# Kernel optimization log

Hardware: AMD Instinct MI355X
Metric: run time of the kernel (lower is better)

Reference implementation:

```python
import jax, jax.numpy as jnp
import numpy as np

N, K, M, H, F = 4, 1024, 1024, 16, 4096
D = M // H  # per-head dim (dim_q = dim_v = 64)
EPS = 1e-5


def _mha(q_in, k_in, v_in, Wq, bq, Wk, bk, Wv, bv, Wo, bo, mask):
    # Wq/Wk/Wv: [H, M, D]; bq/bk/bv: [H, D]; Wo: [H*D, M]; bo: [M]
    q = jnp.einsum('nkm,hmd->nhkd', q_in, Wq) + bq[None, :, None, :]
    k = jnp.einsum('nkm,hmd->nhkd', k_in, Wk) + bk[None, :, None, :]
    v = jnp.einsum('nkm,hmd->nhkd', v_in, Wv) + bv[None, :, None, :]
    scores = jnp.einsum('nhkd,nhld->nhkl', q, k) / jnp.sqrt(jnp.asarray(D, q.dtype))
    if mask is not None:
        scores = jnp.where(mask[:, None, :, :] == 0, jnp.asarray(-jnp.inf, q.dtype), scores)
    attn = jax.nn.softmax(scores, axis=-1)          # [N,H,K,K]
    y = jnp.einsum('nhkl,nhld->nhkd', attn, v)      # [N,H,K,D]
    y = y.transpose(0, 2, 1, 3).reshape(q_in.shape[0], q_in.shape[1], -1)  # concat heads -> [N,K,H*D]
    return y @ Wo + bo


def _ln(x, g, b):
    mu = jnp.mean(x, axis=-1, keepdims=True)
    var = jnp.mean((x - mu) ** 2, axis=-1, keepdims=True)
    return (x - mu) * jax.lax.rsqrt(var + EPS) * g + b


def setup_inputs() -> dict:
    key = jax.random.key(0)
    ks = jax.random.split(key, 24)
    s = 0.02
    def rn(k, shape):
        return jax.random.normal(k, shape, dtype=jnp.float32) * s
    inp = {
        'dec_inp': jax.random.normal(ks[0], (N, K, M), dtype=jnp.float32),
        'enc_out': jax.random.normal(ks[1], (N, K, M), dtype=jnp.float32),
        'mask': jnp.tril(jnp.ones((K, K), dtype=jnp.int32))[None].repeat(N, axis=0),
        # self-attention params
        'Wq_s': rn(ks[2], (H, M, D)), 'bq_s': jnp.zeros((H, D)),
        'Wk_s': rn(ks[3], (H, M, D)), 'bk_s': jnp.zeros((H, D)),
        'Wv_s': rn(ks[4], (H, M, D)), 'bv_s': jnp.zeros((H, D)),
        'Wo_s': rn(ks[5], (H * D, M)), 'bo_s': jnp.zeros((M,)),
        # cross-attention params
        'Wq_c': rn(ks[6], (H, M, D)), 'bq_c': jnp.zeros((H, D)),
        'Wk_c': rn(ks[7], (H, M, D)), 'bk_c': jnp.zeros((H, D)),
        'Wv_c': rn(ks[8], (H, M, D)), 'bv_c': jnp.zeros((H, D)),
        'Wo_c': rn(ks[9], (H * D, M)), 'bo_c': jnp.zeros((M,)),
        # feedforward params
        'W1': rn(ks[10], (M, F)), 'b1': jnp.zeros((F,)),
        'W2': rn(ks[11], (F, M)), 'b2': jnp.zeros((M,)),
        # layernorm params
        'g1': jnp.ones((M,)), 'be1': jnp.zeros((M,)),
        'g2': jnp.ones((M,)), 'be2': jnp.zeros((M,)),
        'g3': jnp.ones((M,)), 'be3': jnp.zeros((M,)),
    }
    return inp


def reference(dec_inp, enc_out, mask,
              Wq_s, bq_s, Wk_s, bk_s, Wv_s, bv_s, Wo_s, bo_s,
              Wq_c, bq_c, Wk_c, bk_c, Wv_c, bv_c, Wo_c, bo_c,
              W1, b1, W2, b2, g1, be1, g2, be2, g3, be3):
    # masked self-attention + residual + LN (dropout = identity in eval)
    out1 = _mha(dec_inp, dec_inp, dec_inp, Wq_s, bq_s, Wk_s, bk_s, Wv_s, bv_s, Wo_s, bo_s, mask)
    out2 = _ln(dec_inp + out1, g1, be1)
    # cross-attention with encoder output + residual + LN
    out3 = _mha(out2, enc_out, enc_out, Wq_c, bq_c, Wk_c, bk_c, Wv_c, bv_c, Wo_c, bo_c, None)
    out4 = _ln(out3 + out2, g2, be2)
    # feedforward + residual + LN
    out5 = jax.nn.relu(out4 @ W1 + b1) @ W2 + b2
    return _ln(out5 + out4, g3, be3)
```

## Files before the change

kernel.cpp:

```cpp
#include <hip/hip_runtime.h>

#define NB   4
#define SEQ  1024
#define MD   1024
#define NH   16
#define HD   64
#define FF   4096
#define NK   (NB*SEQ)
#define EPSF 1e-5f
#define QS   3072

typedef short short8 __attribute__((ext_vector_type(8)));
typedef float f32x4  __attribute__((ext_vector_type(4)));
typedef unsigned short u16;
typedef unsigned int u32;

__device__ __forceinline__ u16 f2bf(float x) {
    union { float f; unsigned u; } v; v.f = x;
    unsigned r = v.u + 0x7FFF + ((v.u >> 16) & 1);
    return (u16)(r >> 16);
}
__device__ __forceinline__ u16 f2bf_trunc(float x) {
    union { float f; unsigned u; } v; v.f = x;
    return (u16)(v.u >> 16);
}
__device__ __forceinline__ float bf2f(u16 x) {
    union { unsigned u; float f; } v; v.u = ((unsigned)x) << 16;
    return v.f;
}
__device__ __forceinline__ void gload_lds16(const void* g, void* l) {
    __builtin_amdgcn_global_load_lds(
        (const __attribute__((address_space(1))) unsigned int*)g,
        (__attribute__((address_space(3))) unsigned int*)l,
        16, 0, 0);
}

__global__ __launch_bounds__(256) void conv_bf16(const float* __restrict__ s0,
                                                 const float* __restrict__ s1,
                                                 u16* __restrict__ d0,
                                                 u16* __restrict__ d1) {
    const float* S = blockIdx.y ? s1 : s0;
    u16* D = blockIdx.y ? d1 : d0;
    const int i = blockIdx.x * 256 + threadIdx.x;
    float4 v = ((const float4*)S)[i];
    ushort4 o;
    o.x = f2bf(v.x); o.y = f2bf(v.y); o.z = f2bf(v.z); o.w = f2bf(v.w);
    ((ushort4*)D)[i] = o;
}

__global__ __launch_bounds__(256) void mask_tiles(const int* __restrict__ mask,
                                                  int* __restrict__ cls,
                                                  u32* __restrict__ bits) {
    const int jt = blockIdx.x, qt = blockIdx.y, n = blockIdx.z;
    const int t = threadIdx.x;
    const int r = t >> 1, h2 = (t & 1) * 2;
    u32 bb[2];
#pragma unroll
    for (int sg = 0; sg < 2; ++sg) {
        const int* mp = &mask[((size_t)n * SEQ + qt * 128 + r) * SEQ + jt * 128 + (h2 + sg) * 32];
        u32 b = 0;
#pragma unroll
        for (int k = 0; k < 8; ++k) {
            int4 v = *(const int4*)(mp + k * 4);
            b |= (v.x ? 1u : 0u) << (k * 4 + 0);
            b |= (v.y ? 1u : 0u) << (k * 4 + 1);
            b |= (v.z ? 1u : 0u) << (k * 4 + 2);
            b |= (v.w ? 1u : 0u) << (k * 4 + 3);
        }
        bb[sg] = b;
    }
    const int tile = (n * 8 + qt) * 8 + jt;
    bits[((size_t)tile * 128 + r) * 4 + h2]     = bb[0];
    bits[((size_t)tile * 128 + r) * 4 + h2 + 1] = bb[1];
    const int nfull  = __syncthreads_count(bb[0] == 0xFFFFFFFFu && bb[1] == 0xFFFFFFFFu);
    const int nempty = __syncthreads_count(bb[0] == 0u && bb[1] == 0u);
    if (t == 0) cls[tile] = (nfull == 256) ? 2 : ((nempty == 256) ? 0 : 1);
}

struct QkvArgs { const float* src[6]; u16* dst[6]; };

__global__ __launch_bounds__(256) void repack_qkv(QkvArgs a) {
    const int m0 = blockIdx.x * 64;
    const int h  = blockIdx.y;
    const int w  = blockIdx.z;
    const float* W = a.src[w];
    u16* BT = a.dst[w];
    const int t = threadIdx.x;
    __shared__ u16 Ts[64][72];

    const int r = t >> 4, c4 = (t & 15) * 4;
#pragma unroll
    for (int p = 0; p < 4; ++p) {
        const int row = r + p * 16;
        float4 v = *(const float4*)&W[((size_t)h * 1024 + m0 + row) * 64 + c4];
        Ts[row][c4] = f2bf(v.x); Ts[row][c4 + 1] = f2bf(v.y);
        Ts[row][c4 + 2] = f2bf(v.z); Ts[row][c4 + 3] = f2bf(v.w);
    }
    __syncthreads();
    const int d = t >> 2, j0 = (t & 3) * 16;
#pragma unroll
    for (int p = 0; p < 4; ++p) {
        ushort4 o;
        o.x = Ts[j0 + p * 4 + 0][d]; o.y = Ts[j0 + p * 4 + 1][d];
        o.z = Ts[j0 + p * 4 + 2][d]; o.w = Ts[j0 + p * 4 + 3][d];
        *(ushort4*)&BT[((size_t)h * 64 + d) * 1024 + m0 + j0 + p * 4] = o;
    }
}

struct FD { const float* src; int ss; u16* dst; int ds; };
struct FlatArgs { FD d[10]; };

__global__ __launch_bounds__(256) void repack_flat(FlatArgs fa) {
    FD u = fa.d[blockIdx.z];
    const int r0 = blockIdx.x * 64;
    const int c0 = blockIdx.y * 64;
    const int t  = threadIdx.x;
    __shared__ u16 Ts[64][72];

    const int r = t >> 4, c4 = (t & 15) * 4;
#pragma unroll
    for (int p = 0; p < 4; ++p) {
        const int row = r + p * 16;
        float4 v = *(const float4*)&u.src[(size_t)(r0 + row) * u.ss + c0 + c4];
        Ts[row][c4] = f2bf(v.x); Ts[row][c4 + 1] = f2bf(v.y);
        Ts[row][c4 + 2] = f2bf(v.z); Ts[row][c4 + 3] = f2bf(v.w);
    }
    __syncthreads();
    const int d = t >> 2, j0 = (t & 3) * 16;
#pragma unroll
    for (int p = 0; p < 4; ++p) {
        ushort4 o;
        o.x = Ts[j0 + p * 4 + 0][d]; o.y = Ts[j0 + p * 4 + 1][d];
        o.z = Ts[j0 + p * 4 + 2][d]; o.w = Ts[j0 + p * 4 + 3][d];
        *(ushort4*)&u.dst[(size_t)(c0 + d) * u.ds + r0 + j0 + p * 4] = o;
    }
}

template<int OUT_BF16, int RELU, int RESID, int BIAS3, int PARTIAL, int VT>
__global__ __launch_bounds__(256) void gemm_mfma(const u16* __restrict__ A,
                                                 const u16* __restrict__ A2,
                                                 int Astride,
                                                 const u16* __restrict__ BT,
                                                 int Bstride,
                                                 const float* __restrict__ b0,
                                                 const float* __restrict__ b1p,
                                                 const float* __restrict__ b2p,
                                                 const float* __restrict__ resid,
                                                 void* __restrict__ Cout,
                                                 u16* __restrict__ VtOut,
                                                 int Kd, int Nd) {
    const int nt = blockIdx.x;
    const int mt = blockIdx.y;
    const int t  = threadIdx.x;
    const int wave = t >> 6, lane = t & 63;
    const int q = lane >> 4, l16 = lane & 15;
    const int wm = wave >> 1, wn = wave & 1;

    __shared__ __align__(16) u16 As[128 * 64];
    __shared__ __align__(16) u16 Bs[128 * 64];

    const int row0 = mt * 128, col0 = nt * 128;
    const u16* Ause = (col0 < 1024) ? A : A2;
    const int kBase = PARTIAL ? blockIdx.z * Kd : 0;

    f32x4 acc[4][4];
#pragma unroll
    for (int r = 0; r < 4; ++r)
#pragma unroll
        for (int c = 0; c < 4; ++c) acc[r][c] = (f32x4)0.0f;

    const int lrow = lane >> 3;
    const int lcb  = lane & 7;

    for (int k0 = 0; k0 < Kd; k0 += 64) {
        __syncthreads();
#pragma unroll
        for (int p = 0; p < 4; ++p) {
            const int rr = wave * 32 + p * 8 + lrow;
            const int gcb = lcb ^ (rr & 7);
            gload_lds16(Ause + (size_t)(row0 + rr) * Astride + kBase + k0 + gcb * 8, As + (size_t)(wave * 32 + p * 8) * 64);
            gload_lds16(BT   + (size_t)(col0 + rr) * Bstride + kBase + k0 + gcb * 8, Bs + (size_t)(wave * 32 + p * 8) * 64);
        }
        __syncthreads();

#pragma unroll
        for (int s = 0; s < 2; ++s) {
            const int pb = (q + s * 4) ^ (l16 & 7);
            short8 af[4], bf[4];
#pragma unroll
            for (int r = 0; r < 4; ++r)
                af[r] = *(const short8*)&As[(wm * 64 + r * 16 + l16) * 64 + pb * 8];
#pragma unroll
            for (int c = 0; c < 4; ++c)
                bf[c] = *(const short8*)&Bs[(wn * 64 + c * 16 + l16) * 64 + pb * 8];
#pragma unroll
            for (int r = 0; r < 4; ++r)
#pragma unroll
                for (int c = 0; c < 4; ++c)
                    acc[r][c] = __builtin_amdgcn_mfma_f32_16x16x32_bf16(af[r], bf[c], acc[r][c], 0, 0, 0);
        }
    }

    float* Pout = PARTIAL ? ((float*)Cout + (size_t)blockIdx.z * NK * Nd) : nullptr;

#pragma unroll
    for (int c = 0; c < 4; ++c) {
        const int col = col0 + wn * 64 + c * 16 + l16;
        float bb = 0.0f;
        if (!PARTIAL) {
            if (BIAS3) {
                const int sec = col >> 10;
                const float* bp = sec == 0 ? b0 : (sec == 1 ? b1p : b2p);
                bb = bp[col & 1023];
            } else {
                bb = b0[col];
            }
        }
#pragma unroll
        for (int r = 0; r < 4; ++r) {
#pragma unroll
            for (int reg = 0; reg < 4; ++reg) {
                const int row = row0 + wm * 64 + r * 16 + q * 4 + reg;
                float v = acc[r][c][reg] + bb;
                if (PARTIAL) {
                    Pout[(size_t)row * Nd + col] = acc[r][c][reg];
                } else {
                    if (RELU)  v = fmaxf(v, 0.0f);
                    if (RESID) v += resid[(size_t)row * Nd + col];
                    if (OUT_BF16) ((u16*)Cout)[(size_t)row * Nd + col] = f2bf(v);
                    else          ((float*)Cout)[(size_t)row * Nd + col] = v;
                }
            }
        }
    }
}

template<int BN, int OUT_BF16, int RELU, int BIAS3, int PARTIAL, int VT>
__global__ __launch_bounds__(512, 2) void gemm256(const u16* __restrict__ A,
                                                  const u16* __restrict__ A2,
                                                  int Astride,
                                                  const u16* __restrict__ BT,
                                                  int Bstride,
                                                  const float* __restrict__ b0,
                                                  const float* __restrict__ b1p,
                                                  const float* __restrict__ b2p,
                                                  void* __restrict__ Cout,
                                                  u16* __restrict__ VtOut,
                                                  int Kd, int Nd, int swzW) {
    const int t  = threadIdx.x;
    const int wave = t >> 6, lane = t & 63;
    const int q = lane >> 4, l16 = lane & 15;
    const int wm = wave >> 2, wn = wave & 3;
    constexpr int NC = BN / 64;

    const int gx = gridDim.x;
    const int bid = blockIdx.x + blockIdx.y * gx;
    const int cpx = (gx * gridDim.y) >> 3;
    const int xcd = bid & 7;
    const int cc  = bid >> 3;
    const int regNX = gx / swzW;
    const int mtspan = cpx / swzW;
    const int nt = (xcd % regNX) * swzW + cc % swzW;
    const int mt = (xcd / regNX) * mtspan + cc / swzW;

    extern __shared__ __align__(16) char smem[];
    u16* As = (u16*)smem;
    u16* Bs = (u16*)(smem + 2 * 256 * 64 * 2);

    const int row0 = mt * 256, col0 = nt * BN;
    const u16* Ause = (col0 < 1024) ? A : A2;
    const int kBase = PARTIAL ? blockIdx.z * Kd : 0;

    f32x4 acc[8][NC];
#pragma unroll
    for (int r = 0; r < 8; ++r)
#pragma unroll
        for (int c = 0; c < NC; ++c) acc[r][c] = (f32x4)0.0f;

    const int lrow = lane >> 3;
    const int lcb  = lane & 7;

    auto stage = [&](int buf, int kk) {
#pragma unroll
        for (int p = 0; p < 4; ++p) {
            const int rr = wave * 32 + p * 8 + lrow;
            const int gcb = lcb ^ (rr & 7);
            gload_lds16(Ause + (size_t)(row0 + rr) * Astride + kk + gcb * 8,
                        As + (size_t)buf * (256 * 64) + (wave * 32 + p * 8) * 64);
        }
#pragma unroll
        for (int p = 0; p < BN / 64; ++p) {
            const int rr = wave * (BN / 8) + p * 8 + lrow;
            const int gcb = lcb ^ (rr & 7);
            gload_lds16(BT + (size_t)(col0 + rr) * Bstride + kk + gcb * 8,
                        Bs + (size_t)buf * (BN * 64) + (wave * (BN / 8) + p * 8) * 64);
        }
    };

    const int nsteps = Kd / 64;
    stage(0, kBase);

    int cur = 0;
    for (int it = 0; it < nsteps; ++it) {
        const bool pre = (it + 1 < nsteps);
        if (pre) {
            stage(cur ^ 1, kBase + (it + 1) * 64);
            if constexpr (BN == 256) asm volatile("s_waitcnt vmcnt(8)" ::: "memory");
            else                     asm volatile("s_waitcnt vmcnt(6)" ::: "memory");
        } else {
            asm volatile("s_waitcnt vmcnt(0)" ::: "memory");
        }
        __builtin_amdgcn_s_barrier();

        const u16* Ab = As + (size_t)cur * (256 * 64);
        const u16* Bb = Bs + (size_t)cur * (BN * 64);
#pragma unroll
        for (int s = 0; s < 2; ++s) {
            const int pb = (q + s * 4) ^ (l16 & 7);
            short8 af[8], bf[NC];
#pragma unroll
            for (int r = 0; r < 8; ++r)
                af[r] = *(const short8*)&Ab[(wm * 128 + r * 16 + l16) * 64 + pb * 8];
#pragma unroll
            for (int c = 0; c < NC; ++c)
                bf[c] = *(const short8*)&Bb[(wn * (BN / 4) + c * 16 + l16) * 64 + pb * 8];
#pragma unroll
            for (int r = 0; r < 8; ++r)
#pragma unroll
                for (int c = 0; c < NC; ++c)
                    acc[r][c] = __builtin_amdgcn_mfma_f32_16x16x32_bf16(af[r], bf[c], acc[r][c], 0, 0, 0);
        }
        __builtin_amdgcn_s_barrier();
        cur ^= 1;
    }

    if (VT && col0 >= 2048) {
#pragma unroll
        for (int c = 0; c < NC; ++c) {
            const int col = col0 + wn * (BN / 4) + c * 16 + l16;
            const float bb = b2p[col & 1023];
            const int d = col & 63, hh = (col >> 6) & 15;
#pragma unroll
            for (int r = 0; r < 8; ++r) {
                const int row = row0 + wm * 128 + r * 16 + q * 4;
                const int nn = row >> 10, k = row & 1023;
                ushort4 o;
                o.x = f2bf(acc[r][c][0] + bb);
                o.y = f2bf(acc[r][c][1] + bb);
                o.z = f2bf(acc[r][c][2] + bb);
                o.w = f2bf(acc[r][c][3] + bb);
                *(ushort4*)&VtOut[((size_t)(nn * 16 + hh) * 64 + d) * 1024 + k] = o;
            }
        }
        return;
    }

    float* Pout = PARTIAL ? ((float*)Cout + (size_t)blockIdx.z * NK * Nd) : nullptr;

#pragma unroll
    for (int c = 0; c < NC; ++c) {
        const int col = col0 + wn * (BN / 4) + c * 16 + l16;
        float bb = 0.0f;
        if (!PARTIAL) {
            if (BIAS3) {
                const int sec = col >> 10;
                const float* bp = sec == 0 ? b0 : (sec == 1 ? b1p : b2p);
                bb = bp[col & 1023];
            } else {
                bb = b0[col];
            }
        }
#pragma unroll
        for (int r = 0; r < 8; ++r) {
#pragma unroll
            for (int reg = 0; reg < 4; ++reg) {
                const int row = row0 + wm * 128 + r * 16 + q * 4 + reg;
                float v = acc[r][c][reg] + bb;
                if (PARTIAL) {
                    Pout[(size_t)row * Nd + col] = acc[r][c][reg];
                } else {
                    if (RELU)  v = fmaxf(v, 0.0f);
                    if (OUT_BF16) ((u16*)Cout)[(size_t)row * Nd + col] = f2bf(v);
                    else          ((float*)Cout)[(size_t)row * Nd + col] = v;
                }
            }
        }
    }
}

#define PSTR 136
#define ATTN_LDS (128*64*2 + 64*128*2 + 8*16*PSTR*2)

__global__ __launch_bounds__(512, 4) void attn_mfma(const u16* __restrict__ QKV,
                                                    const u16* __restrict__ Vt,
                                                    const int* __restrict__ cls,
                                                    const u32* __restrict__ bits,
                                                    u16* __restrict__ Yout) {
    const int qt = blockIdx.x;
    const int h  = blockIdx.y;
    const int n  = blockIdx.z;
    const int t  = threadIdx.x;
    const int wave = t >> 6;
    const int lane = t & 63;
    const int quad = lane >> 4;
    const int l16  = lane & 15;
    const int sw   = wave >> 2;
    const int wq   = wave & 3;

    extern __shared__ __align__(16) char smem[];
    u16* Ks = (u16*)smem;
    u16* Vs = (u16*)(smem + 128 * 64 * 2);
    u16* Pw = (u16*)(smem + 128 * 64 * 2 + 64 * 128 * 2) + wave * 16 * PSTR;

    const int bh = n * NH + h;
    const int i0 = qt * 128;

    int cl[8];
    if (cls) {
        const int* cp = &cls[(n * 8 + qt) * 8];
#pragma unroll
        for (int j = 0; j < 8; ++j) cl[j] = cp[j];
    } else {
#pragma unroll
        for (int j = 0; j < 8; ++j) cl[j] = 2;
    }

    short8 qf[2];
    {
        const u16* qrow = QKV + ((size_t)n * SEQ + i0 + sw * 64 + wq * 16 + l16) * QS + h * 64 + quad * 8;
        short8 a = *(const short8*)(qrow);
        short8 b = *(const short8*)(qrow + 32);
#pragma unroll
        for (int j = 0; j < 8; ++j) {
            qf[0][j] = (short)f2bf(bf2f((u16)a[j]) * 0.18033688f);
            qf[1][j] = (short)f2bf(bf2f((u16)b[j]) * 0.18033688f);
        }
    }

    f32x4 O[4];
#pragma unroll
    for (int d = 0; d < 4; ++d) O[d] = (f32x4)0.0f;
    float lrow[4] = {};

    const int krow = lane >> 3, kblk = lane & 7;
    const int vrow = lane >> 4, vblk = lane & 15;
    const int x7 = l16 & 7;

    for (int jt = 0; jt < SEQ / 128; ++jt) {
        const int c = cl[jt];
        if (c == 0) continue;
        __syncthreads();

#pragma unroll
        for (int p = 0; p < 2; ++p) {
            const int rr = wave * 16 + p * 8 + krow;
            const int kb = kblk ^ (rr & 7);
            gload_lds16(QKV + ((size_t)n * SEQ + jt * 128 + rr) * QS + 1024 + h * 64 + kb * 8,
                        Ks + (wave * 16 + p * 8) * 64);
        }
#pragma unroll
        for (int p = 0; p < 2; ++p) {
            const int rr = wave * 8 + p * 4 + vrow;
            const int kb = vblk ^ (rr & 15);
            gload_lds16(Vt + ((size_t)bh * HD + rr) * SEQ + jt * 128 + kb * 8,
                        Vs + (wave * 8 + p * 4) * 128);
        }
        __syncthreads();

        f32x4 S[8];
#pragma unroll
        for (int sub = 0; sub < 8; ++sub) {
            S[sub] = (f32x4)0.0f;
            const int row = sub * 16 + l16;
            short8 k0 = *(const short8*)&Ks[row * 64 + ((quad ^ x7) * 8)];
            S[sub] = __builtin_amdgcn_mfma_f32_16x16x32_bf16(qf[0], k0, S[sub], 0, 0, 0);
            short8 k1 = *(const short8*)&Ks[row * 64 + (((4 + quad) ^ x7) * 8)];
            S[sub] = __builtin_amdgcn_mfma_f32_16x16x32_bf16(qf[1], k1, S[sub], 0, 0, 0);
        }

        if (c == 1) {
#pragma unroll
            for (int reg = 0; reg < 4; ++reg) {
                const int row = sw * 64 + wq * 16 + quad * 4 + reg;
                const uint4 mm = *(const uint4*)&bits[((size_t)((n * 8 + qt) * 8 + jt) * 128 + row) * 4];
#pragma unroll
                for (int sub = 0; sub < 8; ++sub) {
                    const u32 seg = (sub >> 1) == 0 ? mm.x : (sub >> 1) == 1 ? mm.y : (sub >> 1) == 2 ? mm.z : mm.w;
                    if (!((seg >> ((sub & 1) * 16 + l16)) & 1u)) S[sub][reg] = -1e30f;
                }
            }
        }

#pragma unroll
        for (int reg = 0; reg < 4; ++reg) {
            float rs = 0.0f;
#pragma unroll
            for (int sub = 0; sub < 8; ++sub) {
                float e = exp2f(S[sub][reg]);
                Pw[(quad * 4 + reg) * PSTR + sub * 16 + l16] = f2bf_trunc(e);
                rs += e;
            }
            rs += __shfl_xor(rs, 1);
            rs += __shfl_xor(rs, 2);
            rs += __shfl_xor(rs, 4);
            rs += __shfl_xor(rs, 8);
            lrow[reg] += rs;
        }

        short8 pa[4];
#pragma unroll
        for (int ks = 0; ks < 4; ++ks)
            pa[ks] = *(const short8*)&Pw[l16 * PSTR + ks * 32 + quad * 8];
#pragma unroll
        for (int d = 0; d < 4; ++d) {
            const int row = d * 16 + l16;
#pragma unroll
            for (int ks = 0; ks < 4; ++ks) {
                short8 vb = *(const short8*)&Vs[row * 128 + (((ks * 4 + quad) ^ l16) & 15) * 8];
                O[d] = __builtin_amdgcn_mfma_f32_16x16x32_bf16(pa[ks], vb, O[d], 0, 0, 0);
            }
        }
    }

#pragma unroll
    for (int d = 0; d < 4; ++d) {
#pragma unroll
        for (int reg = 0; reg < 4; ++reg) {
            const int row = i0 + sw * 64 + wq * 16 + quad * 4 + reg;
            const int col = h * 64 + d * 16 + l16;
            Yout[((size_t)n * SEQ + row) * QS + col] = f2bf(O[d][reg] / lrow[reg]);
        }
    }
}

__global__ __launch_bounds__(256) void ln_kernel(const float* __restrict__ X,
                                                 const float* __restrict__ g,
                                                 const float* __restrict__ be,
                                                 float* __restrict__ Y,
                                                 u16* __restrict__ Yb) {
    const int row = blockIdx.x;
    const int t = threadIdx.x;
    __shared__ float red[256];

    const float4 v = ((const float4*)(X + (size_t)row * MD))[t];
    red[t] = v.x + v.y + v.z + v.w;
    __syncthreads();
    for (int s2 = 128; s2 > 0; s2 >>= 1) {
        if (t < s2) red[t] += red[t + s2];
        __syncthreads();
    }
    const float mu = red[0] * (1.0f / MD);
    __syncthreads();

    float dx = v.x - mu, dy = v.y - mu, dz = v.z - mu, dw = v.w - mu;
    red[t] = dx * dx + dy * dy + dz * dz + dw * dw;
    __syncthreads();
    for (int s2 = 128; s2 > 0; s2 >>= 1) {
        if (t < s2) red[t] += red[t + s2];
        __syncthreads();
    }
    const float var = red[0] * (1.0f / MD);
    const float rs = rsqrtf(var + EPSF);

    const float4 gv = ((const float4*)g)[t];
    const float4 bv = ((const float4*)be)[t];
    float4 o;
    o.x = dx * rs * gv.x + bv.x;
    o.y = dy * rs * gv.y + bv.y;
    o.z = dz * rs * gv.z + bv.z;
    o.w = dw * rs * gv.w + bv.w;
    if (Y) ((float4*)(Y + (size_t)row * MD))[t] = o;
    if (Yb) {
        ushort4 ob;
        ob.x = f2bf(o.x); ob.y = f2bf(o.y); ob.z = f2bf(o.z); ob.w = f2bf(o.w);
        ((ushort4*)(Yb + (size_t)row * MD))[t] = ob;
    }
}

__global__ __launch_bounds__(256) void ln_fused2(const float* __restrict__ p0,
                                                 const float* __restrict__ p1,
                                                 const float* __restrict__ bias,
                                                 const float* __restrict__ resid,
                                                 const float* __restrict__ g,
                                                 const float* __restrict__ be,
                                                 float* __restrict__ Y) {
    const int row = blockIdx.x;
    const int t = threadIdx.x;
    __shared__ float red[256];

    const float4 a = ((const float4*)(p0 + (size_t)row * MD))[t];
    const float4 b = ((const float4*)(p1 + (size_t)row * MD))[t];
    const float4 r = ((const float4*)(resid + (size_t)row * MD))[t];
    const float4 bi = ((const float4*)bias)[t];
    float4 v;
    v.x = a.x + b.x + r.x + bi.x;
    v.y = a.y + b.y + r.y + bi.y;
    v.z = a.z + b.z + r.z + bi.z;
    v.w = a.w + b.w + r.w + bi.w;

    red[t] = v.x + v.y + v.z + v.w;
    __syncthreads();
    for (int s2 = 128; s2 > 0; s2 >>= 1) {
        if (t < s2) red[t] += red[t + s2];
        __syncthreads();
    }
    const float mu = red[0] * (1.0f / MD);
    __syncthreads();

    float dx = v.x - mu, dy = v.y - mu, dz = v.z - mu, dw = v.w - mu;
    red[t] = dx * dx + dy * dy + dz * dz + dw * dw;
    __syncthreads();
    for (int s2 = 128; s2 > 0; s2 >>= 1) {
        if (t < s2) red[t] += red[t + s2];
        __syncthreads();
    }
    const float var = red[0] * (1.0f / MD);
    const float rs = rsqrtf(var + EPSF);

    const float4 gv = ((const float4*)g)[t];
    const float4 bv = ((const float4*)be)[t];
    float4 o;
    o.x = dx * rs * gv.x + bv.x;
    o.y = dy * rs * gv.y + bv.y;
    o.z = dz * rs * gv.z + bv.z;
    o.w = dw * rs * gv.w + bv.w;
    ((float4*)(Y + (size_t)row * MD))[t] = o;
}

extern "C" void kernel_launch(void* const* d_in, const int* in_sizes, int n_in,
                              void* d_out, int out_size, void* d_ws, size_t ws_size,
                              hipStream_t stream) {
    const float* dec  = (const float*)d_in[0];
    const float* enc  = (const float*)d_in[1];
    const int*   mask = (const int*)d_in[2];
    const float* Wq_s = (const float*)d_in[3];
    const float* bq_s = (const float*)d_in[4];
    const float* Wk_s = (const float*)d_in[5];
    const float* bk_s = (const float*)d_in[6];
    const float* Wv_s = (const float*)d_in[7];
    const float* bv_s = (const float*)d_in[8];
    const float* Wo_s = (const float*)d_in[9];
    const float* bo_s = (const float*)d_in[10];
    const float* Wq_c = (const float*)d_in[11];
    const float* bq_c = (const float*)d_in[12];
    const float* Wk_c = (const float*)d_in[13];
    const float* bk_c = (const float*)d_in[14];
    const float* Wv_c = (const float*)d_in[15];
    const float* bv_c = (const float*)d_in[16];
    const float* Wo_c = (const float*)d_in[17];
    const float* bo_c = (const float*)d_in[18];
    const float* W1   = (const float*)d_in[19];
    const float* b1   = (const float*)d_in[20];
    const float* W2   = (const float*)d_in[21];
    const float* b2   = (const float*)d_in[22];
    const float* g1   = (const float*)d_in[23];
    const float* be1  = (const float*)d_in[24];
    const float* g2   = (const float*)d_in[25];
    const float* be2  = (const float*)d_in[26];
    const float* g3   = (const float*)d_in[27];
    const float* be3  = (const float*)d_in[28];

    char* wsb = (char*)d_ws;
    const size_t MB = 1u << 20;
    u16*   decb  = (u16*)(wsb + 0 * MB);
    u16*   O2b   = (u16*)(wsb + 0 * MB);
    u16*   encb  = (u16*)(wsb + 8 * MB);
    u16*   O4b   = (u16*)(wsb + 8 * MB);
    u16*   WqkvsT= (u16*)(wsb + 16 * MB);
    u16*   WqkvcT= (u16*)(wsb + 22 * MB);
    u16*   WosT  = (u16*)(wsb + 28 * MB);
    u16*   WocT  = (u16*)(wsb + 30 * MB);
    u16*   W1T   = (u16*)(wsb + 32 * MB);
    u16*   W2T   = (u16*)(wsb + 40 * MB);
    u16*   QKVb  = (u16*)(wsb + 48 * MB);
    u16*   Vt    = (u16*)(wsb + 72 * MB);
    u16*   Hb    = (u16*)(wsb + 48 * MB);
    int*   mcls  = (int*)(wsb + 80 * MB);
    u32*   mbits = (u32*)(wsb + 80 * MB + 64 * 1024);
    float* Tb    = (float*)(wsb + 80 * MB);
    float* FP    = (float*)(wsb + 0 * MB);
    float* O2    = (float*)(wsb + 96 * MB);
    float* O4    = (float*)(wsb + 96 * MB);

    dim3 blk(256);
    dim3 blkA(512);
    dim3 blkG(512);
    dim3 gConv(NK * MD / 4 / 256, 2);
    dim3 gMask(8, 8, 4);
    dim3 gQkvW(16, 16, 6);
    dim3 gFlatW(16, 16, 10);
    dim3 gAttn(SEQ / 128, NH, NB);
    dim3 gQKV(QS / 256, NK / 256);
    dim3 gOut(MD / 128, NK / 128);
    dim3 gF1(FF / 256, NK / 256);
    dim3 gF2(MD / 128, NK / 256, 2);
    const int G256_LDS  = 2 * (256 + 256) * 64 * 2;
    const int G128_LDS  = 2 * (256 + 128) * 64 * 2;

    conv_bf16<<<gConv, blk, 0, stream>>>(dec, enc, decb, encb);
    mask_tiles<<<gMask, blk, 0, stream>>>(mask, mcls, mbits);

    QkvArgs qa;
    qa.src[0] = Wq_s; qa.src[1] = Wk_s; qa.src[2] = Wv_s;
    qa.src[3] = Wq_c; qa.src[4] = Wk_c; qa.src[5] = Wv_c;
    qa.dst[0] = WqkvsT;                 qa.dst[1] = WqkvsT + (size_t)1024 * 1024;
    qa.dst[2] = WqkvsT + (size_t)2048 * 1024;
    qa.dst[3] = WqkvcT;                 qa.dst[4] = WqkvcT + (size_t)1024 * 1024;
    qa.dst[5] = WqkvcT + (size_t)2048 * 1024;
    repack_qkv<<<gQkvW, blk, 0, stream>>>(qa);

    FlatArgs fa;
    fa.d[0] = { Wo_s, 1024, WosT, 1024 };
    fa.d[1] = { Wo_c, 1024, WocT, 1024 };
    for (int u = 0; u < 4; ++u)
        fa.d[2 + u] = { W1 + (size_t)u * 1024, 4096, W1T + (size_t)u * 1024 * 1024, 1024 };
    for (int u = 0; u < 4; ++u)
        fa.d[6 + u] = { W2 + (size_t)u * 1024 * 1024, 1024, W2T + (size_t)u * 1024, 4096 };
    repack_flat<<<gFlatW, blk, 0, stream>>>(fa);

    gemm256<256, 1, 0, 1, 0, 1><<<gQKV, blkG, G256_LDS, stream>>>(decb, decb, MD, WqkvsT, MD, bq_s, bk_s, bv_s, QKVb, Vt, MD, QS, 3);
    attn_mfma<<<gAttn, blkA, ATTN_LDS, stream>>>(QKVb, Vt, mcls, mbits, QKVb);
    gemm_mfma<0, 0, 1, 0, 0, 0><<<gOut, blk, 0, stream>>>(QKVb, QKVb, QS, WosT, MD, bo_s, nullptr, nullptr, dec, Tb, nullptr, MD, MD);
    ln_kernel<<<NK, blk, 0, stream>>>(Tb, g1, be1, O2, O2b);

    gemm256<256, 1, 0, 1, 0, 1><<<gQKV, blkG, G256_LDS, stream>>>(O2b, encb, MD, WqkvcT, MD, bq_c, bk_c, bv_c, QKVb, Vt, MD, QS, 3);
    attn_mfma<<<gAttn, blkA, ATTN_LDS, stream>>>(QKVb, Vt, nullptr, nullptr, QKVb);
    gemm_mfma<0, 0, 1, 0, 0, 0><<<gOut, blk, 0, stream>>>(QKVb, QKVb, QS, WocT, MD, bo_c, nullptr, nullptr, O2, Tb, nullptr, MD, MD);
    ln_kernel<<<NK, blk, 0, stream>>>(Tb, g2, be2, O4, O4b);

    gemm256<256, 1, 1, 0, 0, 0><<<gF1, blkG, G256_LDS, stream>>>(O4b, O4b, MD, W1T, MD, b1, nullptr, nullptr, Hb, nullptr, MD, FF, 4);
    gemm256<128, 0, 0, 0, 1, 0><<<gF2, blkG, G128_LDS, stream>>>(Hb, Hb, FF, W2T, FF, nullptr, nullptr, nullptr, FP, nullptr, FF / 2, MD, 2);
    ln_fused2<<<NK, blk, 0, stream>>>(FP, FP + (size_t)NK * MD, b2, O4, g3, be3, (float*)d_out);
}
```

Before: 351.4 us.

## Rework big GEMM into 256x128 tiles with triple-buffered split-stage pipeline

Replaces the 256x256/256x128 double-buffered GEMM with a fixed 256x128 tile kernel that stages three LDS buffers two k-steps ahead. Each stage load is split into two halves interleaved with the two MFMA sub-steps, and s_setprio raises wave priority around the MFMA blocks. Grids for the QKV and FFN1 GEMMs double in block count and the XCD swizzle widths change to match. The intent is to hide global-load latency and improve MFMA issue. The cost is a smaller per-block tile, so more total loads, plus extra barriers and more LDS per block.

```diff
diff --git a/kernel.cpp b/kernel.cpp
--- a/kernel.cpp
+++ b/kernel.cpp
@@ -235,23 +235,23 @@
     }
 }
 
-template<int BN, int OUT_BF16, int RELU, int BIAS3, int PARTIAL, int VT>
-__global__ __launch_bounds__(512, 2) void gemm256(const u16* __restrict__ A,
-                                                  const u16* __restrict__ A2,
-                                                  int Astride,
-                                                  const u16* __restrict__ BT,
-                                                  int Bstride,
-                                                  const float* __restrict__ b0,
-                                                  const float* __restrict__ b1p,
-                                                  const float* __restrict__ b2p,
-                                                  void* __restrict__ Cout,
-                                                  u16* __restrict__ VtOut,
-                                                  int Kd, int Nd, int swzW) {
+template<int OUT_BF16, int RELU, int BIAS3, int PARTIAL, int VT>
+__global__ __launch_bounds__(512, 2) void gemm256p(const u16* __restrict__ A,
+                                                   const u16* __restrict__ A2,
+                                                   int Astride,
+                                                   const u16* __restrict__ BT,
+                                                   int Bstride,
+                                                   const float* __restrict__ b0,
+                                                   const float* __restrict__ b1p,
+                                                   const float* __restrict__ b2p,
+                                                   void* __restrict__ Cout,
+                                                   u16* __restrict__ VtOut,
+                                                   int Kd, int Nd, int swzW) {
     const int t  = threadIdx.x;
     const int wave = t >> 6, lane = t & 63;
     const int q = lane >> 4, l16 = lane & 15;
-    const int wm = wave >> 2, wn = wave & 3;
-    constexpr int NC = BN / 64;
+    const int wm = wave >> 1, wn = wave & 1;
+    const int x7 = l16 & 7;
 
     const int gx = gridDim.x;
     const int bid = blockIdx.x + blockIdx.y * gx;
@@ -265,84 +265,111 @@
 
     extern __shared__ __align__(16) char smem[];
     u16* As = (u16*)smem;
-    u16* Bs = (u16*)(smem + 2 * 256 * 64 * 2);
-
-    const int row0 = mt * 256, col0 = nt * BN;
+    u16* Bs = (u16*)(smem + 3 * 256 * 64 * 2);
+
+    const int row0 = mt * 256, col0 = nt * 128;
     const u16* Ause = (col0 < 1024) ? A : A2;
     const int kBase = PARTIAL ? blockIdx.z * Kd : 0;
 
-    f32x4 acc[8][NC];
-#pragma unroll
-    for (int r = 0; r < 8; ++r)
-#pragma unroll
-        for (int c = 0; c < NC; ++c) acc[r][c] = (f32x4)0.0f;
+    f32x4 acc[4][4];
+#pragma unroll
+    for (int r = 0; r < 4; ++r)
+#pragma unroll
+        for (int c = 0; c < 4; ++c) acc[r][c] = (f32x4)0.0f;
 
     const int lrow = lane >> 3;
     const int lcb  = lane & 7;
 
-    auto stage = [&](int buf, int kk) {
-#pragma unroll
-        for (int p = 0; p < 4; ++p) {
-            const int rr = wave * 32 + p * 8 + lrow;
+    auto stagePart = [&](int slot, int kk, int part) {
+#pragma unroll
+        for (int p = 0; p < 2; ++p) {
+            const int rr = wave * 32 + (part * 2 + p) * 8 + lrow;
             const int gcb = lcb ^ (rr & 7);
             gload_lds16(Ause + (size_t)(row0 + rr) * Astride + kk + gcb * 8,
-                        As + (size_t)buf * (256 * 64) + (wave * 32 + p * 8) * 64);
-        }
-#pragma unroll
-        for (int p = 0; p < BN / 64; ++p) {
-            const int rr = wave * (BN / 8) + p * 8 + lrow;
+                        As + slot * (256 * 64) + (wave * 32 + (part * 2 + p) * 8) * 64);
+        }
+        {
+            const int rr = wave * 16 + part * 8 + lrow;
             const int gcb = lcb ^ (rr & 7);
             gload_lds16(BT + (size_t)(col0 + rr) * Bstride + kk + gcb * 8,
-                        Bs + (size_t)buf * (BN * 64) + (wave * (BN / 8) + p * 8) * 64);
+                        Bs + slot * (128 * 64) + (wave * 16 + part * 8) * 64);
         }
     };
 
     const int nsteps = Kd / 64;
-    stage(0, kBase);
-
-    int cur = 0;
+    stagePart(0, kBase, 0);      stagePart(0, kBase, 1);
+    stagePart(1, kBase + 64, 0); stagePart(1, kBase + 64, 1);
+
+    int st = 0, st2 = 2;
     for (int it = 0; it < nsteps; ++it) {
-        const bool pre = (it + 1 < nsteps);
-        if (pre) {
-            stage(cur ^ 1, kBase + (it + 1) * 64);
-            if constexpr (BN == 256) asm volatile("s_waitcnt vmcnt(8)" ::: "memory");
-            else                     asm volatile("s_waitcnt vmcnt(6)" ::: "memory");
+        const int kk2 = kBase + (it + 2) * 64;
+        const u16* Ab = As + st * (256 * 64);
+        const u16* Bb = Bs + st * (128 * 64);
+
+        if (it + 2 < nsteps) {
+            stagePart(st2, kk2, 0);
+            asm volatile("s_waitcnt vmcnt(9)" ::: "memory");
+        } else if (it + 1 < nsteps) {
+            asm volatile("s_waitcnt vmcnt(6)" ::: "memory");
         } else {
             asm volatile("s_waitcnt vmcnt(0)" ::: "memory");
         }
         __builtin_amdgcn_s_barrier();
-
-        const u16* Ab = As + (size_t)cur * (256 * 64);
-        const u16* Bb = Bs + (size_t)cur * (BN * 64);
-#pragma unroll
-        for (int s = 0; s < 2; ++s) {
-            const int pb = (q + s * 4) ^ (l16 & 7);
-            short8 af[8], bf[NC];
-#pragma unroll
-            for (int r = 0; r < 8; ++r)
-                af[r] = *(const short8*)&Ab[(wm * 128 + r * 16 + l16) * 64 + pb * 8];
-#pragma unroll
-            for (int c = 0; c < NC; ++c)
-                bf[c] = *(const short8*)&Bb[(wn * (BN / 4) + c * 16 + l16) * 64 + pb * 8];
-#pragma unroll
-            for (int r = 0; r < 8; ++r)
-#pragma unroll
-                for (int c = 0; c < NC; ++c)
+        {
+            const int pb = q ^ x7;
+            short8 af[4], bf[4];
+#pragma unroll
+            for (int r = 0; r < 4; ++r)
+                af[r] = *(const short8*)&Ab[(wm * 64 + r * 16 + l16) * 64 + pb * 8];
+#pragma unroll
+            for (int c = 0; c < 4; ++c)
+                bf[c] = *(const short8*)&Bb[(wn * 64 + c * 16 + l16) * 64 + pb * 8];
+            __builtin_amdgcn_s_setprio(1);
+#pragma unroll
+            for (int r = 0; r < 4; ++r)
+#pragma unroll
+                for (int c = 0; c < 4; ++c)
                     acc[r][c] = __builtin_amdgcn_mfma_f32_16x16x32_bf16(af[r], bf[c], acc[r][c], 0, 0, 0);
+            __builtin_amdgcn_s_setprio(0);
         }
         __builtin_amdgcn_s_barrier();
-        cur ^= 1;
+
+        if (it + 2 < nsteps) stagePart(st2, kk2, 1);
+        {
+            const int pb = (q + 4) ^ x7;
+            short8 af[4], bf[4];
+#pragma unroll
+            for (int r = 0; r < 4; ++r)
+                af[r] = *(const short8*)&Ab[(wm * 64 + r * 16 + l16) * 64 + pb * 8];
+#pragma unroll
+            for (int c = 0; c < 4; ++c)
+                bf[c] = *(const short8*)&Bb[(wn * 64 + c * 16 + l16) * 64 + pb * 8];
+            __builtin_amdgcn_s_barrier();
+            asm volatile("s_waitcnt lgkmcnt(0)" ::: "memory");
+            __builtin_amdgcn_sched_barrier(0);
+            __builtin_amdgcn_s_setprio(1);
+#pragma unroll
+            for (int r = 0; r < 4; ++r)
+#pragma unroll
+                for (int c = 0; c < 4; ++c)
+                    acc[r][c] = __builtin_amdgcn_mfma_f32_16x16x32_bf16(af[r], bf[c], acc[r][c], 0, 0, 0);
+            __builtin_amdgcn_s_setprio(0);
+        }
+        __builtin_amdgcn_s_barrier();
+
+        st  = (st  == 2) ? 0 : st + 1;
+        st2 = (st2 == 2) ? 0 : st2 + 1;
     }
 
     if (VT && col0 >= 2048) {
 #pragma unroll
-        for (int c = 0; c < NC; ++c) {
-            const int col = col0 + wn * (BN / 4) + c * 16 + l16;
+        for (int c = 0; c < 4; ++c) {
+            const int col = col0 + wn * 64 + c * 16 + l16;
             const float bb = b2p[col & 1023];
             const int d = col & 63, hh = (col >> 6) & 15;
 #pragma unroll
-            for (int r = 0; r < 8; ++r) {
-                const int row = row0 + wm * 128 + r * 16 + q * 4;
+            for (int r = 0; r < 4; ++r) {
+                const int row = row0 + wm * 64 + r * 16 + q * 4;
                 const int nn = row >> 10, k = row & 1023;
                 ushort4 o;
                 o.x = f2bf(acc[r][c][0] + bb);
@@ -358,8 +385,8 @@
     float* Pout = PARTIAL ? ((float*)Cout + (size_t)blockIdx.z * NK * Nd) : nullptr;
 
 #pragma unroll
-    for (int c = 0; c < NC; ++c) {
-        const int col = col0 + wn * (BN / 4) + c * 16 + l16;
+    for (int c = 0; c < 4; ++c) {
+        const int col = col0 + wn * 64 + c * 16 + l16;
         float bb = 0.0f;
         if (!PARTIAL) {
             if (BIAS3) {
@@ -371,10 +398,10 @@
             }
         }
 #pragma unroll
-        for (int r = 0; r < 8; ++r) {
+        for (int r = 0; r < 4; ++r) {
 #pragma unroll
             for (int reg = 0; reg < 4; ++reg) {
-                const int row = row0 + wm * 128 + r * 16 + q * 4 + reg;
+                const int row = row0 + wm * 64 + r * 16 + q * 4 + reg;
                 float v = acc[r][c][reg] + bb;
                 if (PARTIAL) {
                     Pout[(size_t)row * Nd + col] = acc[r][c][reg];
@@ -690,12 +717,11 @@
     dim3 gQkvW(16, 16, 6);
     dim3 gFlatW(16, 16, 10);
     dim3 gAttn(SEQ / 128, NH, NB);
-    dim3 gQKV(QS / 256, NK / 256);
+    dim3 gQKV(QS / 128, NK / 256);
     dim3 gOut(MD / 128, NK / 128);
-    dim3 gF1(FF / 256, NK / 256);
+    dim3 gF1(FF / 128, NK / 256);
     dim3 gF2(MD / 128, NK / 256, 2);
-    const int G256_LDS  = 2 * (256 + 256) * 64 * 2;
-    const int G128_LDS  = 2 * (256 + 128) * 64 * 2;
+    const int GP_LDS = 3 * (256 * 64 + 128 * 64) * 2;
 
     conv_bf16<<<gConv, blk, 0, stream>>>(dec, enc, decb, encb);
     mask_tiles<<<gMask, blk, 0, stream>>>(mask, mcls, mbits);
@@ -718,17 +744,17 @@
         fa.d[6 + u] = { W2 + (size_t)u * 1024 * 1024, 1024, W2T + (size_t)u * 1024, 4096 };
     repack_flat<<<gFlatW, blk, 0, stream>>>(fa);
 
-    gemm256<256, 1, 0, 1, 0, 1><<<gQKV, blkG, G256_LDS, stream>>>(decb, decb, MD, WqkvsT, MD, bq_s, bk_s, bv_s, QKVb, Vt, MD, QS, 3);
+    gemm256p<1, 0, 1, 0, 1><<<gQKV, blkG, GP_LDS, stream>>>(decb, decb, MD, WqkvsT, MD, bq_s, bk_s, bv_s, QKVb, Vt, MD, QS, 6);
     attn_mfma<<<gAttn, blkA, ATTN_LDS, stream>>>(QKVb, Vt, mcls, mbits, QKVb);
     gemm_mfma<0, 0, 1, 0, 0, 0><<<gOut, blk, 0, stream>>>(QKVb, QKVb, QS, WosT, MD, bo_s, nullptr, nullptr, dec, Tb, nullptr, MD, MD);
     ln_kernel<<<NK, blk, 0, stream>>>(Tb, g1, be1, O2, O2b);
 
-    gemm256<256, 1, 0, 1, 0, 1><<<gQKV, blkG, G256_LDS, stream>>>(O2b, encb, MD, WqkvcT, MD, bq_c, bk_c, bv_c, QKVb, Vt, MD, QS, 3);
+    gemm256p<1, 0, 1, 0, 1><<<gQKV, blkG, GP_LDS, stream>>>(O2b, encb, MD, WqkvcT, MD, bq_c, bk_c, bv_c, QKVb, Vt, MD, QS, 6);
     attn_mfma<<<gAttn, blkA, ATTN_LDS, stream>>>(QKVb, Vt, nullptr, nullptr, QKVb);
     gemm_mfma<0, 0, 1, 0, 0, 0><<<gOut, blk, 0, stream>>>(QKVb, QKVb, QS, WocT, MD, bo_c, nullptr, nullptr, O2, Tb, nullptr, MD, MD);
     ln_kernel<<<NK, blk, 0, stream>>>(Tb, g2, be2, O4, O4b);
 
-    gemm256<256, 1, 1, 0, 0, 0><<<gF1, blkG, G256_LDS, stream>>>(O4b, O4b, MD, W1T, MD, b1, nullptr, nullptr, Hb, nullptr, MD, FF, 4);
-    gemm256<128, 0, 0, 0, 1, 0><<<gF2, blkG, G128_LDS, stream>>>(Hb, Hb, FF, W2T, FF, nullptr, nullptr, nullptr, FP, nullptr, FF / 2, MD, 2);
+    gemm256p<1, 1, 0, 0, 0><<<gF1, blkG, GP_LDS, stream>>>(O4b, O4b, MD, W1T, MD, b1, nullptr, nullptr, Hb, nullptr, MD, FF, 8);
+    gemm256p<0, 0, 0, 1, 0><<<gF2, blkG, GP_LDS, stream>>>(Hb, Hb, FF, W2T, FF, nullptr, nullptr, nullptr, FP, nullptr, FF / 2, MD, 2);
     ln_fused2<<<NK, blk, 0, stream>>>(FP, FP + (size_t)NK * MD, b2, O4, g3, be3, (float*)d_out);
 }
```

Result: slower. 362.7 us, median of 2 (+3.2%).
